# Optimization experiments

Hardware: AMD Instinct MI355X
Metric: run time of the kernel (lower is better)

Reference implementation:

```python
import jax, jax.numpy as jnp
import numpy as np

HID = 128          # hidden_channels
NL = 3             # num_layers
K = 60             # sort-pool k
NG = 128           # number of graphs in the batch
NPG = 1024         # nodes per graph
N = NG * NPG       # 131072 total nodes
E = N * 16         # 2097152 edges
MAXZ = 1000        # z embedding vocab
D_TOT = HID * NL + 1  # 385 = total_latent_dim = conv1 kernel = conv1 stride
C1, C2 = 16, 32    # conv1d channels
KW2 = 5            # conv2 kernel
DENSE = ((K - 2) // 2 + 1 - KW2 + 1) * C2  # 832


def setup_inputs() -> dict:
    key = jax.random.key(0)
    ks = jax.random.split(key, 24)
    inp = {
        'z': jax.random.randint(ks[0], (N,), 0, MAXZ),
        'src': jax.random.randint(ks[1], (E,), 0, N),
        'dst': jax.random.randint(ks[2], (E,), 0, N),
        'edge_weight': jax.random.uniform(ks[3], (E,), dtype=jnp.float32),
        'z_emb': jax.random.normal(ks[4], (MAXZ, HID), dtype=jnp.float32) * 0.02,
    }
    # GraphConv weights: 128->128, 128->128, 128->128, 128->1
    dims = [(HID, HID), (HID, HID), (HID, HID), (HID, 1)]
    for i, (di, do) in enumerate(dims):
        inp[f'W{i}'] = jax.random.normal(ks[5 + i], (di, do), dtype=jnp.float32) / np.sqrt(di)
        inp[f'b{i}'] = jnp.zeros((do,), dtype=jnp.float32)
    inp['conv1_w'] = jax.random.normal(ks[10], (C1, D_TOT), dtype=jnp.float32) / np.sqrt(D_TOT)
    inp['conv1_b'] = jnp.zeros((C1,), dtype=jnp.float32)
    inp['conv2_w'] = jax.random.normal(ks[11], (C2, C1, KW2), dtype=jnp.float32) / np.sqrt(C1 * KW2)
    inp['conv2_b'] = jnp.zeros((C2,), dtype=jnp.float32)
    inp['lin1_w'] = jax.random.normal(ks[12], (DENSE, 128), dtype=jnp.float32) / np.sqrt(DENSE)
    inp['lin1_b'] = jnp.zeros((128,), dtype=jnp.float32)
    inp['lin2_w'] = jax.random.normal(ks[13], (128, 1), dtype=jnp.float32) / np.sqrt(128)
    inp['lin2_b'] = jnp.zeros((1,), dtype=jnp.float32)
    return inp


def _forward(z, src, dst, edge_weight, z_emb,
             W0, b0, W1, b1, W2, b2, W3, b3,
             conv1_w, conv1_b, conv2_w, conv2_b,
             lin1_w, lin1_b, lin2_w, lin2_b):
    ones = jnp.ones((E,), dtype=jnp.float32)
    out_deg = jnp.clip(jax.ops.segment_sum(ones, src, num_segments=N), 1.0)
    in_deg = jnp.clip(jax.ops.segment_sum(ones, dst, num_segments=N), 1.0)
    norm_s = out_deg ** -0.5  # DGL GraphConv norm='both'
    norm_d = in_deg ** -0.5

    def gconv(x, W, b):
        # linear transform first (equivalent math, smaller edge traffic for last layer)
        h = (x * norm_s[:, None]) @ W            # [N, out]
        m = h[src] * edge_weight[:, None]         # gather over edges [E, out]
        agg = jax.ops.segment_sum(m, dst, num_segments=N)  # scatter-add [N, out]
        return agg * norm_d[:, None] + b

    h = z_emb[z]                                  # [N, HID]
    xs = []
    for W, b in ((W0, b0), (W1, b1), (W2, b2), (W3, b3)):
        h = jnp.tanh(gconv(h, W, b))
        xs.append(h)
    feat = jnp.concatenate(xs, axis=-1)           # [N, 385]

    # DGL SortPooling: sort each node's channels ascending, then per-graph top-k by last channel
    feat = jnp.sort(feat, axis=-1)
    fg = feat.reshape(NG, NPG, D_TOT)
    _, idx = jax.lax.top_k(fg[..., -1], K)        # descending, [NG, K]
    pooled = jnp.take_along_axis(fg, idx[..., None], axis=1)  # [NG, K, D_TOT]

    # conv1: Conv1d(1, 16, kernel=D_TOT, stride=D_TOT) on [NG,1,K*D_TOT] == per-window matmul
    h1 = jax.nn.relu(jnp.einsum('gkd,cd->gck', pooled, conv1_w) + conv1_b[None, :, None])  # [NG,16,K]
    h1 = h1.reshape(NG, C1, K // 2, 2).max(axis=-1)  # MaxPool1d(2,2) -> [NG,16,K//2]
    h2 = jax.lax.conv_general_dilated(h1, conv2_w, window_strides=(1,), padding='VALID')
    h2 = jax.nn.relu(h2 + conv2_b[None, :, None])    # [NG,32,K//2-4]
    flat = h2.reshape(NG, -1)                        # [NG, 832]
    h3 = jax.nn.relu(flat @ lin1_w + lin1_b)
    # dropout p=0.5 is identity in eval mode
    return h3 @ lin2_w + lin2_b                      # [NG, 1]


def reference(z, src, dst, edge_weight, z_emb,
              W0, b0, W1, b1, W2, b2, W3, b3,
              conv1_w, conv1_b, conv2_w, conv2_b,
              lin1_w, lin1_b, lin2_w, lin2_b):
    return _forward(z, src, dst, edge_weight, z_emb,
                    W0, b0, W1, b1, W2, b2, W3, b3,
                    conv1_w, conv1_b, conv2_w, conv2_b,
                    lin1_w, lin1_b, lin2_w, lin2_b)
```

## Files before the change

kernel.cpp:

```cpp
#include <hip/hip_runtime.h>

#define NN 131072
#define NE 2097152
#define NG 128
#define KTOP 60
#define DTOT 385


__global__ void zero2_k(int* __restrict__ p) {
  p[blockIdx.x * 256 + threadIdx.x] = 0;
}

__global__ void count_k(const int* __restrict__ src, const int* __restrict__ dst,
                        int* __restrict__ cs, int* __restrict__ cd) {
  int e = blockIdx.x * 256 + threadIdx.x;
  atomicAdd(&cs[src[e]], 1);
  atomicAdd(&cd[dst[e]], 1);
}

__global__ void norm_k(const int* __restrict__ cs, const int* __restrict__ cd,
                       float* __restrict__ ns, float* __restrict__ nd) {
  int n = blockIdx.x * 256 + threadIdx.x;
  int a = cs[n]; a = a < 1 ? 1 : a;
  int b = cd[n]; b = b < 1 ? 1 : b;
  ns[n] = 1.0f / sqrtf((float)a);
  nd[n] = 1.0f / sqrtf((float)b);
}

__global__ void scan1_k(const int* __restrict__ cnt, int* __restrict__ out,
                        int* __restrict__ partials) {
  __shared__ int ts[256];
  int t = threadIdx.x;
  int base = blockIdx.x * 1024 + t * 4;
  int v0 = cnt[base], v1 = cnt[base + 1], v2 = cnt[base + 2], v3 = cnt[base + 3];
  int s = v0 + v1 + v2 + v3;
  int x = s;
  ts[t] = x;
  __syncthreads();
  for (int off = 1; off < 256; off <<= 1) {
    int y = (t >= off) ? ts[t - off] : 0;
    __syncthreads();
    x += y; ts[t] = x;
    __syncthreads();
  }
  int excl = x - s;
  out[base]     = excl;
  out[base + 1] = excl + v0;
  out[base + 2] = excl + v0 + v1;
  out[base + 3] = excl + v0 + v1 + v2;
  if (t == 255) partials[blockIdx.x] = x;
}

__global__ void scan2_k(int* __restrict__ partials) {
  __shared__ int a[128];
  int t = threadIdx.x;
  int v = partials[t];
  int x = v; a[t] = x;
  __syncthreads();
  for (int off = 1; off < 128; off <<= 1) {
    int y = (t >= off) ? a[t - off] : 0;
    __syncthreads();
    x += y; a[t] = x;
    __syncthreads();
  }
  partials[t] = x - v;
}

__global__ void scan3_k(int* __restrict__ csr_off, const int* __restrict__ partials,
                        int* __restrict__ cursor) {
  int add = partials[blockIdx.x];
  int base = blockIdx.x * 1024 + threadIdx.x * 4;
  for (int i = 0; i < 4; ++i) {
    int v = csr_off[base + i] + add;
    csr_off[base + i] = v;
    cursor[base + i]  = v;
  }
  if (blockIdx.x == 0 && threadIdx.x == 0) csr_off[NN] = NE;
}

__global__ void fill_k(const int* __restrict__ src, const int* __restrict__ dst,
                       const float* __restrict__ ew, const float* __restrict__ ns,
                       int* __restrict__ cursor, int2* __restrict__ csr) {
  int e = blockIdx.x * 256 + threadIdx.x;
  int s = src[e];
  int d = dst[e];
  int slot = atomicAdd(&cursor[d], 1);
  csr[slot] = make_int2(s, __float_as_int(ew[e] * ns[s]));
}


__global__ void agg0_k(const int* __restrict__ z, const float* __restrict__ zemb,
                       const int* __restrict__ off, const int2* __restrict__ csr,
                       float* __restrict__ t) {
  int n = (blockIdx.x * 256 + threadIdx.x) >> 6;
  int lane = threadIdx.x & 63;
  int h = lane >> 5, q = lane & 31;
  int jb = off[n], je = off[n + 1];
  float4 s0 = {0, 0, 0, 0}, s1 = {0, 0, 0, 0};
  const float4* e4 = (const float4*)zemb;
  int j = jb + h;
  for (; j + 2 < je; j += 4) {
    int2 pa = csr[j], pb = csr[j + 2];
    float4 ha = e4[(size_t)z[pa.x] * 32 + q];
    float4 hb = e4[(size_t)z[pb.x] * 32 + q];
    float wa = __int_as_float(pa.y), wb = __int_as_float(pb.y);
    s0.x += ha.x * wa; s0.y += ha.y * wa; s0.z += ha.z * wa; s0.w += ha.w * wa;
    s1.x += hb.x * wb; s1.y += hb.y * wb; s1.z += hb.z * wb; s1.w += hb.w * wb;
  }
  if (j < je) {
    int2 pa = csr[j];
    float4 ha = e4[(size_t)z[pa.x] * 32 + q];
    float wa = __int_as_float(pa.y);
    s0.x += ha.x * wa; s0.y += ha.y * wa; s0.z += ha.z * wa; s0.w += ha.w * wa;
  }
  float4 s = {s0.x + s1.x, s0.y + s1.y, s0.z + s1.z, s0.w + s1.w};
  s.x += __shfl_xor(s.x, 32);
  s.y += __shfl_xor(s.y, 32);
  s.z += __shfl_xor(s.z, 32);
  s.w += __shfl_xor(s.w, 32);
  if (h == 0) ((float4*)t)[(size_t)n * 32 + q] = s;
}

__global__ void aggx_k(const float* __restrict__ x, const int* __restrict__ off,
                       const int2* __restrict__ csr, float* __restrict__ t) {
  int n = (blockIdx.x * 256 + threadIdx.x) >> 6;
  int lane = threadIdx.x & 63;
  int h = lane >> 5, q = lane & 31;
  int jb = off[n], je = off[n + 1];
  float4 s0 = {0, 0, 0, 0}, s1 = {0, 0, 0, 0};
  const float4* x4 = (const float4*)x;
  int j = jb + h;
  for (; j + 2 < je; j += 4) {
    int2 pa = csr[j], pb = csr[j + 2];
    float4 ha = x4[(size_t)pa.x * 32 + q];
    float4 hb = x4[(size_t)pb.x * 32 + q];
    float wa = __int_as_float(pa.y), wb = __int_as_float(pb.y);
    s0.x += ha.x * wa; s0.y += ha.y * wa; s0.z += ha.z * wa; s0.w += ha.w * wa;
    s1.x += hb.x * wb; s1.y += hb.y * wb; s1.z += hb.z * wb; s1.w += hb.w * wb;
  }
  if (j < je) {
    int2 pa = csr[j];
    float4 ha = x4[(size_t)pa.x * 32 + q];
    float wa = __int_as_float(pa.y);
    s0.x += ha.x * wa; s0.y += ha.y * wa; s0.z += ha.z * wa; s0.w += ha.w * wa;
  }
  float4 s = {s0.x + s1.x, s0.y + s1.y, s0.z + s1.z, s0.w + s1.w};
  s.x += __shfl_xor(s.x, 32);
  s.y += __shfl_xor(s.y, 32);
  s.z += __shfl_xor(s.z, 32);
  s.w += __shfl_xor(s.w, 32);
  if (h == 0) ((float4*)t)[(size_t)n * 32 + q] = s;
}

__device__ __forceinline__ void fma4(float4& acc, float s, const float4 w) {
  acc.x += s * w.x; acc.y += s * w.y; acc.z += s * w.z; acc.w += s * w.w;
}

__global__ void gemm_inplace_k(float* __restrict__ buf, const float* __restrict__ nd,
                               const float* __restrict__ W, const float* __restrict__ bias,
                               float* __restrict__ rowmax) {
  __shared__ float xt[64 * 128];
  const int t = threadIdx.x;
  const int rowBase = blockIdx.x * 64;
  float4* xt4 = (float4*)xt;
  const float4* g4 = (const float4*)(buf + (size_t)rowBase * 128);
  for (int i = t; i < 2048; i += 256) xt4[i] = g4[i];
  __syncthreads();
  const int w  = t >> 6;
  const int l  = t & 63;
  const int c4 = l & 31;
  const int rh = l >> 5;
  const int r0 = w * 16 + rh * 8;
  float4 acc[8];
#pragma unroll
  for (int r = 0; r < 8; ++r) acc[r] = {0, 0, 0, 0};
  const float4* W4 = (const float4*)W;
  for (int k4 = 0; k4 < 32; ++k4) {
    float4 xv[8];
#pragma unroll
    for (int r = 0; r < 8; ++r) xv[r] = xt4[(r0 + r) * 32 + k4];
    const float4 w0 = W4[(k4 * 4 + 0) * 32 + c4];
    const float4 w1 = W4[(k4 * 4 + 1) * 32 + c4];
    const float4 w2 = W4[(k4 * 4 + 2) * 32 + c4];
    const float4 w3 = W4[(k4 * 4 + 3) * 32 + c4];
#pragma unroll
    for (int r = 0; r < 8; ++r) {
      fma4(acc[r], xv[r].x, w0);
      fma4(acc[r], xv[r].y, w1);
      fma4(acc[r], xv[r].z, w2);
      fma4(acc[r], xv[r].w, w3);
    }
  }
  const float4 bb = ((const float4*)bias)[c4];
#pragma unroll
  for (int r = 0; r < 8; ++r) {
    const int row = rowBase + r0 + r;
    const float s = nd[row];
    float4 o;
    o.x = tanhf(acc[r].x * s + bb.x);
    o.y = tanhf(acc[r].y * s + bb.y);
    o.z = tanhf(acc[r].z * s + bb.z);
    o.w = tanhf(acc[r].w * s + bb.w);
    ((float4*)(buf + (size_t)row * 128))[c4] = o;
    float m = fmaxf(fmaxf(o.x, o.y), fmaxf(o.z, o.w));
    for (int d = 16; d; d >>= 1) m = fmaxf(m, __shfl_xor(m, d));
    if (c4 == 0) rowmax[row] = m;
  }
}

__global__ void gemv_y2_k(const float* __restrict__ x, const float* __restrict__ W3,
                          float* __restrict__ y2) {
  __shared__ float w[128];
  if (threadIdx.x < 128) w[threadIdx.x] = W3[threadIdx.x];
  __syncthreads();
  int lane = threadIdx.x & 63, wv = threadIdx.x >> 6;
  int n = blockIdx.x * 4 + wv;
  const float* xr = x + (size_t)n * 128;
  float p = xr[lane] * w[lane] + xr[lane + 64] * w[lane + 64];
  for (int o = 32; o; o >>= 1) p += __shfl_down(p, o);
  if (lane == 0) y2[n] = p;
}

__global__ void agg3s_k(const float* __restrict__ y2, const int* __restrict__ off,
                        const int2* __restrict__ csr, const float* __restrict__ nd,
                        const float* __restrict__ b3, float* __restrict__ xs3) {
  int n = blockIdx.x * 256 + threadIdx.x;
  int jb = off[n], je = off[n + 1];
  float a0 = 0.f, a1 = 0.f;
  int j = jb;
  for (; j + 1 < je; j += 2) {
    int2 pa = csr[j], pb = csr[j + 1];
    a0 += __int_as_float(pa.y) * y2[pa.x];
    a1 += __int_as_float(pb.y) * y2[pb.x];
  }
  if (j < je) {
    int2 pa = csr[j];
    a0 += __int_as_float(pa.y) * y2[pa.x];
  }
  xs3[n] = tanhf((a0 + a1) * nd[n] + b3[0]);
}


__global__ void nodemax_small_k(const float* __restrict__ rm0, const float* __restrict__ rm1,
                                const float* __restrict__ rm2, const float* __restrict__ xs3,
                                float* __restrict__ nmax) {
  int n = blockIdx.x * 256 + threadIdx.x;
  nmax[n] = fmaxf(fmaxf(rm0[n], rm1[n]), fmaxf(rm2[n], xs3[n]));
}

__global__ void topk_k(const float* __restrict__ nmax, int* __restrict__ sel) {
  __shared__ float v[1024];
  __shared__ int ix[1024];
  int g = blockIdx.x, t = threadIdx.x;
  for (int i = t; i < 1024; i += 512) { v[i] = nmax[(size_t)g * 1024 + i]; ix[i] = i; }
  __syncthreads();
  for (int k = 2; k <= 1024; k <<= 1) {
    for (int j = k >> 1; j > 0; j >>= 1) {
      int i = ((t & ~(j - 1)) << 1) | (t & (j - 1));
      int pj = i | j;
      bool up = ((i & k) == 0);
      float va = v[i], vb = v[pj];
      int ia = ix[i], ib = ix[pj];
      bool b_bef_a = (vb > va) || (vb == va && ib < ia);
      bool a_bef_b = (va > vb) || (va == vb && ia < ib);
      bool sw = up ? b_bef_a : a_bef_b;
      if (sw) { v[i] = vb; v[pj] = va; ix[i] = ib; ix[pj] = ia; }
      __syncthreads();
    }
  }
  if (t < KTOP) sel[g * KTOP + t] = g * 1024 + ix[t];
}

__global__ void sortpool_k(const int* __restrict__ sel, const float* __restrict__ xs0,
                           const float* __restrict__ xs1, const float* __restrict__ xs2,
                           const float* __restrict__ xs3, float* __restrict__ pooled) {
  __shared__ float sv[512];
  int blk = blockIdx.x, t = threadIdx.x;
  int node = sel[blk];
  const float inf = __int_as_float(0x7f800000);
  for (int i = t; i < 512; i += 256) {
    float val;
    if (i < 128)      val = xs0[(size_t)node * 128 + i];
    else if (i < 256) val = xs1[(size_t)node * 128 + (i - 128)];
    else if (i < 384) val = xs2[(size_t)node * 128 + (i - 256)];
    else if (i == 384) val = xs3[node];
    else val = inf;
    sv[i] = val;
  }
  __syncthreads();
  for (int k = 2; k <= 512; k <<= 1) {
    for (int j = k >> 1; j > 0; j >>= 1) {
      int i = ((t & ~(j - 1)) << 1) | (t & (j - 1));
      int pj = i | j;
      bool up = ((i & k) == 0);
      float a = sv[i], b = sv[pj];
      if (up ? (a > b) : (a < b)) { sv[i] = b; sv[pj] = a; }
      __syncthreads();
    }
  }
  for (int i = t; i < DTOT; i += 256) pooled[(size_t)blk * DTOT + i] = sv[i];
}


__global__ void head_k(const float* __restrict__ pooled,
                       const float* __restrict__ c1w, const float* __restrict__ c1b,
                       const float* __restrict__ c2w, const float* __restrict__ c2b,
                       const float* __restrict__ l1w, const float* __restrict__ l1b,
                       const float* __restrict__ l2w, const float* __restrict__ l2b,
                       float* __restrict__ out) {
  __shared__ float h1[16 * 60];
  __shared__ float h1p[16 * 30];
  __shared__ float h2f[832];
  __shared__ float h3[128];
  int g = blockIdx.x, t = threadIdx.x;
  const float* pg = pooled + (size_t)g * KTOP * DTOT;
  for (int oi = t; oi < 960; oi += 256) {
    int c = oi & 15, kk = oi >> 4;
    const float* pr = pg + kk * DTOT;
    const float* wr = c1w + c * DTOT;
    float s = c1b[c];
    for (int d = 0; d < DTOT; ++d) s += pr[d] * wr[d];
    h1[c * 60 + kk] = fmaxf(s, 0.f);
  }
  __syncthreads();
  for (int i = t; i < 480; i += 256) {
    int c = i / 30, j = i % 30;
    h1p[c * 30 + j] = fmaxf(h1[c * 60 + 2 * j], h1[c * 60 + 2 * j + 1]);
  }
  __syncthreads();
  for (int i = t; i < 832; i += 256) {
    int oc = i / 26, x = i % 26;
    float s = c2b[oc];
    for (int ic = 0; ic < 16; ++ic)
#pragma unroll
      for (int w = 0; w < 5; ++w)
        s += h1p[ic * 30 + x + w] * c2w[oc * 80 + ic * 5 + w];
    h2f[i] = fmaxf(s, 0.f);
  }
  __syncthreads();
  if (t < 128) {
    float s = l1b[t];
    for (int d = 0; d < 832; ++d) s += h2f[d] * l1w[d * 128 + t];
    h3[t] = fmaxf(s, 0.f);
  }
  __syncthreads();
  if (t < 64) {
    float p = h3[t] * l2w[t] + h3[t + 64] * l2w[t + 64];
    for (int o = 32; o; o >>= 1) p += __shfl_down(p, o);
    if (t == 0) out[g] = p + l2b[0];
  }
}


extern "C" void kernel_launch(void* const* d_in, const int* in_sizes, int n_in,
                              void* d_out, int out_size, void* d_ws, size_t ws_size,
                              hipStream_t stream) {
  const int* z = (const int*)d_in[0];
  const int* src = (const int*)d_in[1];
  const int* dst = (const int*)d_in[2];
  const float* ew = (const float*)d_in[3];
  const float* zemb = (const float*)d_in[4];
  const float* W0 = (const float*)d_in[5];  const float* b0 = (const float*)d_in[6];
  const float* W1 = (const float*)d_in[7];  const float* b1 = (const float*)d_in[8];
  const float* W2 = (const float*)d_in[9];  const float* b2 = (const float*)d_in[10];
  const float* W3 = (const float*)d_in[11]; const float* b3 = (const float*)d_in[12];
  const float* c1w = (const float*)d_in[13]; const float* c1b = (const float*)d_in[14];
  const float* c2w = (const float*)d_in[15]; const float* c2b = (const float*)d_in[16];
  const float* l1w = (const float*)d_in[17]; const float* l1b = (const float*)d_in[18];
  const float* l2w = (const float*)d_in[19]; const float* l2b = (const float*)d_in[20];
  float* out = (float*)d_out;

  char* ws = (char*)d_ws;
  size_t off = 0;
  auto alloc = [&](size_t bytes) {
    void* p = ws + off;
    off += (bytes + 255) & ~(size_t)255;
    return p;
  };
  int*   cnt     = (int*)alloc((size_t)2 * NN * 4);
  float* norm_s  = (float*)alloc((size_t)NN * 4);
  float* norm_d  = (float*)alloc((size_t)NN * 4);
  int*   csr_off = (int*)alloc((size_t)(NN + 1) * 4);
  int*   cursor  = (int*)alloc((size_t)NN * 4);
  int*   partials= (int*)alloc(1024);
  int2*  csr     = (int2*)alloc((size_t)NE * 8);
  float* xs0     = (float*)alloc((size_t)NN * 128 * 4);
  float* xs1     = (float*)alloc((size_t)NN * 128 * 4);
  float* xs2     = (float*)alloc((size_t)NN * 128 * 4);
  float* xs3     = (float*)alloc((size_t)NN * 4);
  float* y2      = (float*)alloc((size_t)NN * 4);
  float* rm0     = (float*)alloc((size_t)NN * 4);
  float* rm1     = (float*)alloc((size_t)NN * 4);
  float* rm2     = (float*)alloc((size_t)NN * 4);
  float* nmax    = (float*)alloc((size_t)NN * 4);
  int*   sel     = (int*)alloc((size_t)NG * KTOP * 4);
  float* pooled  = (float*)alloc((size_t)NG * KTOP * DTOT * 4);
  (void)in_sizes; (void)n_in; (void)out_size;
  if (ws_size < off) return;

  int* cnt_s = cnt;
  int* cnt_d = cnt + NN;

  zero2_k<<<2 * NN / 256, 256, 0, stream>>>(cnt);
  count_k<<<NE / 256, 256, 0, stream>>>(src, dst, cnt_s, cnt_d);
  norm_k<<<NN / 256, 256, 0, stream>>>(cnt_s, cnt_d, norm_s, norm_d);
  scan1_k<<<128, 256, 0, stream>>>(cnt_d, csr_off, partials);
  scan2_k<<<1, 128, 0, stream>>>(partials);
  scan3_k<<<128, 256, 0, stream>>>(csr_off, partials, cursor);
  fill_k<<<NE / 256, 256, 0, stream>>>(src, dst, ew, norm_s, cursor, csr);

  agg0_k<<<NN * 64 / 256, 256, 0, stream>>>(z, zemb, csr_off, csr, xs0);
  gemm_inplace_k<<<NN / 64, 256, 0, stream>>>(xs0, norm_d, W0, b0, rm0);
  aggx_k<<<NN * 64 / 256, 256, 0, stream>>>(xs0, csr_off, csr, xs1);
  gemm_inplace_k<<<NN / 64, 256, 0, stream>>>(xs1, norm_d, W1, b1, rm1);
  aggx_k<<<NN * 64 / 256, 256, 0, stream>>>(xs1, csr_off, csr, xs2);
  gemm_inplace_k<<<NN / 64, 256, 0, stream>>>(xs2, norm_d, W2, b2, rm2);

  gemv_y2_k<<<NN / 4, 256, 0, stream>>>(xs2, W3, y2);
  agg3s_k<<<NN / 256, 256, 0, stream>>>(y2, csr_off, csr, norm_d, b3, xs3);

  nodemax_small_k<<<NN / 256, 256, 0, stream>>>(rm0, rm1, rm2, xs3, nmax);
  topk_k<<<NG, 512, 0, stream>>>(nmax, sel);
  sortpool_k<<<NG * KTOP, 256, 0, stream>>>(sel, xs0, xs1, xs2, xs3, pooled);

  head_k<<<NG, 256, 0, stream>>>(pooled, c1w, c1b, c2w, c2b, l1w, l1b, l2w, l2b, out);
}
```

Measured before the change: 1.184 ms.

## Build CSR via two-level bucket partition with shared-memory histograms

Replaces the global atomic degree counting, three-kernel scan and atomic CSR fill with a two-pass bucket partition. Edges are first binned into 128 buckets of 1024 nodes using shared-memory histograms. Per-bucket blocks then compute in-degree and out-degree, offsets, normalisation and CSR placement with shared-memory atomics. This aims to cut scattered global atomics and random writes, but the CSR build now runs on only 128 blocks, each handling about 16K edges, which may limit parallelism. The packing assumes node ids fit in 17 bits, and the edge buffers are aliased into xs0 before it is written.

```diff
diff --git a/kernel.cpp b/kernel.cpp
--- a/kernel.cpp
+++ b/kernel.cpp
@@ -5,87 +5,148 @@
 #define NG 128
 #define KTOP 60
 #define DTOT 385
-
-
-__global__ void zero2_k(int* __restrict__ p) {
-  p[blockIdx.x * 256 + threadIdx.x] = 0;
-}
-
-__global__ void count_k(const int* __restrict__ src, const int* __restrict__ dst,
-                        int* __restrict__ cs, int* __restrict__ cd) {
-  int e = blockIdx.x * 256 + threadIdx.x;
-  atomicAdd(&cs[src[e]], 1);
-  atomicAdd(&cd[dst[e]], 1);
-}
-
-__global__ void norm_k(const int* __restrict__ cs, const int* __restrict__ cd,
-                       float* __restrict__ ns, float* __restrict__ nd) {
-  int n = blockIdx.x * 256 + threadIdx.x;
-  int a = cs[n]; a = a < 1 ? 1 : a;
-  int b = cd[n]; b = b < 1 ? 1 : b;
-  ns[n] = 1.0f / sqrtf((float)a);
-  nd[n] = 1.0f / sqrtf((float)b);
-}
-
-__global__ void scan1_k(const int* __restrict__ cnt, int* __restrict__ out,
-                        int* __restrict__ partials) {
-  __shared__ int ts[256];
+#define EPB 2048
+
+
+__global__ void zero_small_k(int* __restrict__ p, int n) {
+  int i = blockIdx.x * 256 + threadIdx.x;
+  if (i < n) p[i] = 0;
+}
+
+__global__ void bucketcnt_k(const int* __restrict__ src, const int* __restrict__ dst,
+                            int* __restrict__ gd, int* __restrict__ gs) {
+  __shared__ int hd[128], hs[128];
   int t = threadIdx.x;
-  int base = blockIdx.x * 1024 + t * 4;
-  int v0 = cnt[base], v1 = cnt[base + 1], v2 = cnt[base + 2], v3 = cnt[base + 3];
-  int s = v0 + v1 + v2 + v3;
-  int x = s;
-  ts[t] = x;
-  __syncthreads();
-  for (int off = 1; off < 256; off <<= 1) {
-    int y = (t >= off) ? ts[t - off] : 0;
+  if (t < 128) { hd[t] = 0; hs[t] = 0; }
+  __syncthreads();
+  int base = blockIdx.x * EPB;
+#pragma unroll
+  for (int i = 0; i < EPB / 256; ++i) {
+    int e = base + i * 256 + t;
+    atomicAdd(&hd[dst[e] >> 10], 1);
+    atomicAdd(&hs[src[e] >> 10], 1);
+  }
+  __syncthreads();
+  if (t < 128) { atomicAdd(&gd[t], hd[t]); atomicAdd(&gs[t], hs[t]); }
+}
+
+__global__ void bucketscan_k(const int* __restrict__ gd, const int* __restrict__ gs,
+                             int* __restrict__ offd, int* __restrict__ offs,
+                             int* __restrict__ curd, int* __restrict__ curs,
+                             int* __restrict__ csr_off) {
+  __shared__ int a[128], b[128];
+  int t = threadIdx.x;
+  int vd = gd[t], vs = gs[t];
+  int xd = vd, xs = vs;
+  a[t] = xd; b[t] = xs;
+  __syncthreads();
+  for (int o = 1; o < 128; o <<= 1) {
+    int yd = (t >= o) ? a[t - o] : 0;
+    int ys = (t >= o) ? b[t - o] : 0;
     __syncthreads();
-    x += y; ts[t] = x;
+    xd += yd; xs += ys; a[t] = xd; b[t] = xs;
     __syncthreads();
   }
-  int excl = x - s;
-  out[base]     = excl;
-  out[base + 1] = excl + v0;
-  out[base + 2] = excl + v0 + v1;
-  out[base + 3] = excl + v0 + v1 + v2;
-  if (t == 255) partials[blockIdx.x] = x;
-}
-
-__global__ void scan2_k(int* __restrict__ partials) {
-  __shared__ int a[128];
+  offd[t] = xd - vd; offs[t] = xs - vs;
+  curd[t] = xd - vd; curs[t] = xs - vs;
+  if (t == 0) { offd[128] = NE; offs[128] = NE; csr_off[NN] = NE; }
+}
+
+__global__ void part_k(const int* __restrict__ src, const int* __restrict__ dst,
+                       const float* __restrict__ ew,
+                       int* __restrict__ curd, int* __restrict__ curs,
+                       uint2* __restrict__ ebuf, int* __restrict__ sbuf) {
+  __shared__ int hd[128], hs[128], bd[128], bs[128];
   int t = threadIdx.x;
-  int v = partials[t];
-  int x = v; a[t] = x;
-  __syncthreads();
-  for (int off = 1; off < 128; off <<= 1) {
-    int y = (t >= off) ? a[t - off] : 0;
+  if (t < 128) { hd[t] = 0; hs[t] = 0; }
+  __syncthreads();
+  int base = blockIdx.x * EPB;
+  int s[8], d[8], rd[8], rs[8]; float w[8];
+#pragma unroll
+  for (int i = 0; i < 8; ++i) {
+    int e = base + i * 256 + t;
+    s[i] = src[e]; d[i] = dst[e]; w[i] = ew[e];
+    rd[i] = atomicAdd(&hd[d[i] >> 10], 1);
+    rs[i] = atomicAdd(&hs[s[i] >> 10], 1);
+  }
+  __syncthreads();
+  if (t < 128) {
+    bd[t] = atomicAdd(&curd[t], hd[t]);
+    bs[t] = atomicAdd(&curs[t], hs[t]);
+  }
+  __syncthreads();
+#pragma unroll
+  for (int i = 0; i < 8; ++i) {
+    int bind = d[i] >> 10;
+    unsigned packed = (unsigned)s[i] | ((unsigned)(d[i] & 1023) << 17);
+    ebuf[bd[bind] + rd[i]] = make_uint2(packed, __float_as_uint(w[i]));
+    sbuf[bs[s[i] >> 10] + rs[i]] = s[i];
+  }
+}
+
+__global__ void outdeg_k(const int* __restrict__ sbuf, const int* __restrict__ offs,
+                         float* __restrict__ norm_s) {
+  __shared__ int h[1024];
+  int g = blockIdx.x, t = threadIdx.x;
+  for (int i = t; i < 1024; i += 256) h[i] = 0;
+  __syncthreads();
+  int jb = offs[g], je = offs[g + 1];
+  for (int j = jb + t; j < je; j += 256) atomicAdd(&h[sbuf[j] & 1023], 1);
+  __syncthreads();
+  for (int i = t; i < 1024; i += 256) {
+    int c = h[i]; c = c < 1 ? 1 : c;
+    norm_s[g * 1024 + i] = 1.0f / sqrtf((float)c);
+  }
+}
+
+__global__ void csrbuild_k(const uint2* __restrict__ ebuf, const int* __restrict__ offd,
+                           const float* __restrict__ norm_s,
+                           int* __restrict__ csr_off, float* __restrict__ norm_d,
+                           int2* __restrict__ csr) {
+  __shared__ int hist[1024];
+  __shared__ int excl[1024];
+  __shared__ int part[256];
+  int g = blockIdx.x, t = threadIdx.x;
+  for (int i = t; i < 1024; i += 256) hist[i] = 0;
+  __syncthreads();
+  int jb = offd[g], je = offd[g + 1];
+  for (int j = jb + t; j < je; j += 256) atomicAdd(&hist[ebuf[j].x >> 17], 1);
+  __syncthreads();
+  int h0 = hist[4 * t], h1 = hist[4 * t + 1], h2 = hist[4 * t + 2], h3 = hist[4 * t + 3];
+  int sum = h0 + h1 + h2 + h3;
+  int x = sum;
+  part[t] = x;
+  __syncthreads();
+  for (int o = 1; o < 256; o <<= 1) {
+    int y = (t >= o) ? part[t - o] : 0;
     __syncthreads();
-    x += y; a[t] = x;
+    x += y; part[t] = x;
     __syncthreads();
   }
-  partials[t] = x - v;
-}
-
-__global__ void scan3_k(int* __restrict__ csr_off, const int* __restrict__ partials,
-                        int* __restrict__ cursor) {
-  int add = partials[blockIdx.x];
-  int base = blockIdx.x * 1024 + threadIdx.x * 4;
-  for (int i = 0; i < 4; ++i) {
-    int v = csr_off[base + i] + add;
-    csr_off[base + i] = v;
-    cursor[base + i]  = v;
-  }
-  if (blockIdx.x == 0 && threadIdx.x == 0) csr_off[NN] = NE;
-}
-
-__global__ void fill_k(const int* __restrict__ src, const int* __restrict__ dst,
-                       const float* __restrict__ ew, const float* __restrict__ ns,
-                       int* __restrict__ cursor, int2* __restrict__ csr) {
-  int e = blockIdx.x * 256 + threadIdx.x;
-  int s = src[e];
-  int d = dst[e];
-  int slot = atomicAdd(&cursor[d], 1);
-  csr[slot] = make_int2(s, __float_as_int(ew[e] * ns[s]));
+  int e0 = x - sum;
+  excl[4 * t]     = e0;
+  excl[4 * t + 1] = e0 + h0;
+  excl[4 * t + 2] = e0 + h0 + h1;
+  excl[4 * t + 3] = e0 + h0 + h1 + h2;
+  int nb = g * 1024;
+  csr_off[nb + 4 * t]     = jb + e0;
+  csr_off[nb + 4 * t + 1] = jb + e0 + h0;
+  csr_off[nb + 4 * t + 2] = jb + e0 + h0 + h1;
+  csr_off[nb + 4 * t + 3] = jb + e0 + h0 + h1 + h2;
+  int c;
+  c = h0 < 1 ? 1 : h0; norm_d[nb + 4 * t]     = 1.0f / sqrtf((float)c);
+  c = h1 < 1 ? 1 : h1; norm_d[nb + 4 * t + 1] = 1.0f / sqrtf((float)c);
+  c = h2 < 1 ? 1 : h2; norm_d[nb + 4 * t + 2] = 1.0f / sqrtf((float)c);
+  c = h3 < 1 ? 1 : h3; norm_d[nb + 4 * t + 3] = 1.0f / sqrtf((float)c);
+  __syncthreads();
+  for (int j = jb + t; j < je; j += 256) {
+    uint2 e = ebuf[j];
+    int srcn = e.x & 0x1FFFF;
+    int dl = e.x >> 17;
+    float w = __uint_as_float(e.y) * norm_s[srcn];
+    int slot = atomicAdd(&excl[dl], 1);
+    csr[jb + slot] = make_int2(srcn, __float_as_int(w));
+  }
 }
 
 
@@ -377,12 +438,14 @@
     off += (bytes + 255) & ~(size_t)255;
     return p;
   };
-  int*   cnt     = (int*)alloc((size_t)2 * NN * 4);
+  int*   gcnt    = (int*)alloc(256 * 4);
+  int*   offd    = (int*)alloc(129 * 4);
+  int*   offs    = (int*)alloc(129 * 4);
+  int*   curd    = (int*)alloc(128 * 4);
+  int*   curs    = (int*)alloc(128 * 4);
+  int*   csr_off = (int*)alloc((size_t)(NN + 1) * 4);
   float* norm_s  = (float*)alloc((size_t)NN * 4);
   float* norm_d  = (float*)alloc((size_t)NN * 4);
-  int*   csr_off = (int*)alloc((size_t)(NN + 1) * 4);
-  int*   cursor  = (int*)alloc((size_t)NN * 4);
-  int*   partials= (int*)alloc(1024);
   int2*  csr     = (int2*)alloc((size_t)NE * 8);
   float* xs0     = (float*)alloc((size_t)NN * 128 * 4);
   float* xs1     = (float*)alloc((size_t)NN * 128 * 4);
@@ -398,16 +461,17 @@
   (void)in_sizes; (void)n_in; (void)out_size;
   if (ws_size < off) return;
 
-  int* cnt_s = cnt;
-  int* cnt_d = cnt + NN;
-
-  zero2_k<<<2 * NN / 256, 256, 0, stream>>>(cnt);
-  count_k<<<NE / 256, 256, 0, stream>>>(src, dst, cnt_s, cnt_d);
-  norm_k<<<NN / 256, 256, 0, stream>>>(cnt_s, cnt_d, norm_s, norm_d);
-  scan1_k<<<128, 256, 0, stream>>>(cnt_d, csr_off, partials);
-  scan2_k<<<1, 128, 0, stream>>>(partials);
-  scan3_k<<<128, 256, 0, stream>>>(csr_off, partials, cursor);
-  fill_k<<<NE / 256, 256, 0, stream>>>(src, dst, ew, norm_s, cursor, csr);
+  int* gd = gcnt;
+  int* gs = gcnt + 128;
+  uint2* ebuf = (uint2*)xs0;
+  int*   sbuf = (int*)(xs0 + (size_t)NE * 2);
+
+  zero_small_k<<<1, 256, 0, stream>>>(gcnt, 256);
+  bucketcnt_k<<<NE / EPB, 256, 0, stream>>>(src, dst, gd, gs);
+  bucketscan_k<<<1, 128, 0, stream>>>(gd, gs, offd, offs, curd, curs, csr_off);
+  part_k<<<NE / EPB, 256, 0, stream>>>(src, dst, ew, curd, curs, ebuf, sbuf);
+  outdeg_k<<<NG, 256, 0, stream>>>(sbuf, offs, norm_s);
+  csrbuild_k<<<NG, 256, 0, stream>>>(ebuf, offd, norm_s, csr_off, norm_d, csr);
 
   agg0_k<<<NN * 64 / 256, 256, 0, stream>>>(z, zemb, csr_off, csr, xs0);
   gemm_inplace_k<<<NN / 64, 256, 0, stream>>>(xs0, norm_d, W0, b0, rm0);
```

Result: faster. 1.051 ms (-11.3%).
